# Optimization experiments

Hardware: AMD Instinct MI355X
Metric: run time of the kernel (lower is better)

Reference implementation:

```python
import jax, jax.numpy as jnp
import numpy as np

D = 768
H = 8
DH = D // H
SCALE = DH ** -0.5


def layer_norm(x, g, b, eps=1e-5):
    mu = jnp.mean(x, axis=-1, keepdims=True)
    var = jnp.var(x, axis=-1, keepdims=True)
    return (x - mu) * jax.lax.rsqrt(var + eps) * g + b


def setup_inputs() -> dict:
    key = jax.random.key(0)
    ks = jax.random.split(key, 8)
    B, N = 8, 1024
    s = lambda fan_in: 1.0 / np.sqrt(fan_in)
    return {
        "x": jax.random.normal(ks[0], (B, N, D), jnp.float32),
        "w_qkv": jax.random.normal(ks[1], (D, 3 * D), jnp.float32) * s(D),
        "w_o": jax.random.normal(ks[2], (D, D), jnp.float32) * s(D),
        "b_o": jnp.zeros((D,), jnp.float32),
        "w1": jax.random.normal(ks[3], (D, 4 * D), jnp.float32) * s(D),
        "b1": jnp.zeros((4 * D,), jnp.float32),
        "w2": jax.random.normal(ks[4], (4 * D, D), jnp.float32) * s(4 * D),
        "b2": jnp.zeros((D,), jnp.float32),
        "g1": jnp.ones((D,), jnp.float32), "be1": jnp.zeros((D,), jnp.float32),
        "gm": jnp.ones((D,), jnp.float32), "bm": jnp.zeros((D,), jnp.float32),
        "g3": jnp.ones((D,), jnp.float32), "be3": jnp.zeros((D,), jnp.float32),
    }


def reference(x, w_qkv, w_o, b_o, w1, b1, w2, b2, g1, be1, gm, bm, g3, be3):
    B, N, _ = x.shape
    # --- attention branch (pre-norm) ---
    h = layer_norm(x, g1, be1)
    qkv = h @ w_qkv                                   # (B,N,3D)
    qkv = qkv.reshape(B, N, 3, H, DH).transpose(2, 0, 3, 1, 4)  # (3,B,H,N,Dh)
    q, k, v = qkv[0], qkv[1], qkv[2]
    att = jax.nn.softmax(jnp.einsum('bhnd,bhmd->bhnm', q, k) * SCALE, axis=-1)
    o = jnp.einsum('bhnm,bhmd->bhnd', att, v)         # (B,H,N,Dh)
    # faithful to original: reshape WITHOUT transposing heads back
    o = o.reshape(B, N, D)
    o = o @ w_o + b_o
    x = o + x
    # --- MLP branch (has its own pre-norm; GELU after BOTH linears; dropout off) ---
    h = layer_norm(x, gm, bm)
    h = jax.nn.gelu(h @ w1 + b1, approximate=False)
    h = jax.nn.gelu(h @ w2 + b2, approximate=False)
    x = h + x
    return layer_norm(x, g3, be3)
```

## Files before the change

### kernel.cpp

```cpp
#include <hip/hip_runtime.h>
#include <cmath>
#include <cstdint>

typedef __bf16 bf16;
typedef __bf16 bf16x8 __attribute__((ext_vector_type(8)));
typedef __bf16 bf16x4 __attribute__((ext_vector_type(4)));
typedef float  f32x4  __attribute__((ext_vector_type(4)));

#define M_TOK 8192
#define SCALE_ 0.10206207261596575f

__device__ __forceinline__ void gld_lds16(const void* g, void* l) {
  __builtin_amdgcn_global_load_lds(
      (__attribute__((address_space(1))) void*)(uintptr_t)g,
      (__attribute__((address_space(3))) void*)(uintptr_t)l,
      16, 0, 0);
}

__device__ __forceinline__ float gelu_f(float x) {
  float u = x * (0.7978845608f + 0.0356774081f * x * x);
  float t = 1.0f - 2.0f / (__expf(2.0f * u) + 1.0f);
  return 0.5f * x * (1.0f + t);
}

__global__ __launch_bounds__(256) void transpose_cast_all_kernel(
    const float* __restrict__ w_qkv, const float* __restrict__ w_o,
    const float* __restrict__ w1, const float* __restrict__ w2,
    bf16* __restrict__ wqkvT, bf16* __restrict__ woT, bf16* __restrict__ w1T,
    bf16* __restrict__ w2T) {
  __shared__ float tile[32][33];
  int g = blockIdx.x;
  const float* src;
  bf16* dst;
  int K, N, base, xt;
  if (g < 1728) {
    src = w_qkv; dst = wqkvT; K = 768; N = 2304; base = 0; xt = 72;
  } else if (g < 2304) {
    src = w_o; dst = woT; K = 768; N = 768; base = 1728; xt = 24;
  } else if (g < 4608) {
    src = w1; dst = w1T; K = 768; N = 3072; base = 2304; xt = 96;
  } else {
    src = w2; dst = w2T; K = 3072; N = 768; base = 4608; xt = 24;
  }
  int lid = g - base;
  int nt = (lid % xt) * 32, kt = (lid / xt) * 32;
  int tx = threadIdx.x, ty = threadIdx.y;
#pragma unroll
  for (int i = ty; i < 32; i += 8)
    tile[i][tx] = src[(size_t)(kt + i) * N + nt + tx];
  __syncthreads();
#pragma unroll
  for (int i = ty; i < 32; i += 8)
    dst[(size_t)(nt + i) * K + kt + tx] = (bf16)tile[tx][i];
}

__global__ __launch_bounds__(256) void ln_kernel(
    const float* __restrict__ x, const float* __restrict__ g,
    const float* __restrict__ b, bf16* __restrict__ ob) {
  int w = threadIdx.x >> 6, lane = threadIdx.x & 63;
  size_t row = (size_t)blockIdx.x * 4 + w;
  const float* xr = x + row * 768;
  float4 v[3];
  float s = 0.f, sq = 0.f;
#pragma unroll
  for (int k = 0; k < 3; k++) {
    v[k] = *(const float4*)(xr + (k * 64 + lane) * 4);
    s += v[k].x + v[k].y + v[k].z + v[k].w;
    sq += v[k].x * v[k].x + v[k].y * v[k].y + v[k].z * v[k].z + v[k].w * v[k].w;
  }
#pragma unroll
  for (int off = 32; off >= 1; off >>= 1) {
    s += __shfl_xor(s, off);
    sq += __shfl_xor(sq, off);
  }
  float mean = s * (1.f / 768.f);
  float rstd = rsqrtf(sq * (1.f / 768.f) - mean * mean + 1e-5f);
#pragma unroll
  for (int k = 0; k < 3; k++) {
    int c = (k * 64 + lane) * 4;
    float4 gg = *(const float4*)(g + c);
    float4 bb = *(const float4*)(b + c);
    bf16x4 pk = {(bf16)((v[k].x - mean) * rstd * gg.x + bb.x),
                 (bf16)((v[k].y - mean) * rstd * gg.y + bb.y),
                 (bf16)((v[k].z - mean) * rstd * gg.z + bb.z),
                 (bf16)((v[k].w - mean) * rstd * gg.w + bb.w)};
    *(bf16x4*)(ob + row * 768 + c) = pk;
  }
}

__global__ __launch_bounds__(256) void ln2_reduce_kernel(
    const bf16* __restrict__ p, const float* __restrict__ bo,
    const float* __restrict__ xres, const float* __restrict__ g,
    const float* __restrict__ b, bf16* __restrict__ x2,
    bf16* __restrict__ h2) {
  int w = threadIdx.x >> 6, lane = threadIdx.x & 63;
  size_t row = (size_t)blockIdx.x * 4 + w;
  const bf16* p0 = p + row * 768;
  const bf16* p1 = p0 + (size_t)M_TOK * 768;
  const float* xr = xres + row * 768;
  float4 v[3];
  float s = 0.f, sq = 0.f;
#pragma unroll
  for (int k = 0; k < 3; k++) {
    int c = (k * 64 + lane) * 4;
    bf16x4 a0 = *(const bf16x4*)(p0 + c);
    bf16x4 a1 = *(const bf16x4*)(p1 + c);
    float4 bb = *(const float4*)(bo + c);
    float4 rr = *(const float4*)(xr + c);
    v[k].x = (float)a0[0] + (float)a1[0] + bb.x + rr.x;
    v[k].y = (float)a0[1] + (float)a1[1] + bb.y + rr.y;
    v[k].z = (float)a0[2] + (float)a1[2] + bb.z + rr.z;
    v[k].w = (float)a0[3] + (float)a1[3] + bb.w + rr.w;
    bf16x4 xo = {(bf16)v[k].x, (bf16)v[k].y, (bf16)v[k].z, (bf16)v[k].w};
    *(bf16x4*)(x2 + row * 768 + c) = xo;
    s += v[k].x + v[k].y + v[k].z + v[k].w;
    sq += v[k].x * v[k].x + v[k].y * v[k].y + v[k].z * v[k].z + v[k].w * v[k].w;
  }
#pragma unroll
  for (int off = 32; off >= 1; off >>= 1) {
    s += __shfl_xor(s, off);
    sq += __shfl_xor(sq, off);
  }
  float mean = s * (1.f / 768.f);
  float rstd = rsqrtf(sq * (1.f / 768.f) - mean * mean + 1e-5f);
#pragma unroll
  for (int k = 0; k < 3; k++) {
    int c = (k * 64 + lane) * 4;
    float4 gg = *(const float4*)(g + c);
    float4 bb = *(const float4*)(b + c);
    bf16x4 pk = {(bf16)((v[k].x - mean) * rstd * gg.x + bb.x),
                 (bf16)((v[k].y - mean) * rstd * gg.y + bb.y),
                 (bf16)((v[k].z - mean) * rstd * gg.z + bb.z),
                 (bf16)((v[k].w - mean) * rstd * gg.w + bb.w)};
    *(bf16x4*)(h2 + row * 768 + c) = pk;
  }
}

__global__ __launch_bounds__(256) void ln3_reduce_kernel(
    const bf16* __restrict__ p, const float* __restrict__ b2,
    const bf16* __restrict__ x2, const float* __restrict__ g,
    const float* __restrict__ b, float* __restrict__ out) {
  int w = threadIdx.x >> 6, lane = threadIdx.x & 63;
  size_t row = (size_t)blockIdx.x * 4 + w;
  const bf16* p0 = p + row * 768;
  const bf16* p1 = p0 + (size_t)M_TOK * 768;
  const bf16* xr = x2 + row * 768;
  float4 v[3];
  float s = 0.f, sq = 0.f;
#pragma unroll
  for (int k = 0; k < 3; k++) {
    int c = (k * 64 + lane) * 4;
    bf16x4 a0 = *(const bf16x4*)(p0 + c);
    bf16x4 a1 = *(const bf16x4*)(p1 + c);
    float4 bb = *(const float4*)(b2 + c);
    bf16x4 rr = *(const bf16x4*)(xr + c);
    v[k].x = gelu_f((float)a0[0] + (float)a1[0] + bb.x) + (float)rr[0];
    v[k].y = gelu_f((float)a0[1] + (float)a1[1] + bb.y) + (float)rr[1];
    v[k].z = gelu_f((float)a0[2] + (float)a1[2] + bb.z) + (float)rr[2];
    v[k].w = gelu_f((float)a0[3] + (float)a1[3] + bb.w) + (float)rr[3];
    s += v[k].x + v[k].y + v[k].z + v[k].w;
    sq += v[k].x * v[k].x + v[k].y * v[k].y + v[k].z * v[k].z + v[k].w * v[k].w;
  }
#pragma unroll
  for (int off = 32; off >= 1; off >>= 1) {
    s += __shfl_xor(s, off);
    sq += __shfl_xor(sq, off);
  }
  float mean = s * (1.f / 768.f);
  float rstd = rsqrtf(sq * (1.f / 768.f) - mean * mean + 1e-5f);
#pragma unroll
  for (int k = 0; k < 3; k++) {
    int c = (k * 64 + lane) * 4;
    float4 gg = *(const float4*)(g + c);
    float4 bb = *(const float4*)(b + c);
    float4 ov = {(v[k].x - mean) * rstd * gg.x + bb.x,
                 (v[k].y - mean) * rstd * gg.y + bb.y,
                 (v[k].z - mean) * rstd * gg.z + bb.z,
                 (v[k].w - mean) * rstd * gg.w + bb.w};
    *(float4*)(out + row * 768 + c) = ov;
  }
}

template <int EPI, int LDA, int LDB, int KSL, int NN>
__global__ __launch_bounds__(256) void gemm_bt_kernel(
    const bf16* __restrict__ A, const bf16* __restrict__ Bt,
    const float* __restrict__ bias, bf16* __restrict__ outb,
    bf16* __restrict__ qo, bf16* __restrict__ ko, bf16* __restrict__ vto) {
  __shared__ __align__(16) bf16 As[2][128 * 32];
  __shared__ __align__(16) bf16 Bs[2][128 * 32];
  int tid = threadIdx.x;
  int wave = tid >> 6, lane = tid & 63;
  int qd = lane >> 4, lr = lane & 15;
  int bm0 = blockIdx.y * 128, bn0 = blockIdx.x * 128;
  int wm = (wave >> 1) * 64, wn = (wave & 1) * 64;
  int kbase = blockIdx.z * KSL;

  f32x4 acc[4][4] = {};

  int srow = lane >> 2;
  int scol = ((lane & 3) ^ ((lane >> 3) & 3)) * 8;
  const bf16* Ag = A + (size_t)(bm0 + wave * 32 + srow) * LDA + kbase + scol;
  const bf16* Ag2 = Ag + (size_t)16 * LDA;
  const bf16* Bg = Bt + (size_t)(bn0 + wave * 32 + srow) * LDB + kbase + scol;
  const bf16* Bg2 = Bg + (size_t)16 * LDB;
  int rk = (lr >> 1) & 3;

  auto stage = [&](int k0, int buf) {
    char* Al = (char*)As[buf] + wave * 2048;
    char* Bl = (char*)Bs[buf] + wave * 2048;
    gld_lds16(Ag + k0, Al);
    gld_lds16(Ag2 + k0, Al + 1024);
    gld_lds16(Bg + k0, Bl);
    gld_lds16(Bg2 + k0, Bl + 1024);
  };

  stage(0, 0);
  int cur = 0;
#pragma unroll 4
  for (int k0 = 0; k0 < KSL; k0 += 32) {
    __syncthreads();
    if (k0 + 32 < KSL) stage(k0 + 32, cur ^ 1);
    const bf16* Asr = As[cur];
    const bf16* Bsr = Bs[cur];
    bf16x8 af[4], bfv[4];
#pragma unroll
    for (int i = 0; i < 4; i++)
      af[i] = *(const bf16x8*)&Asr[(wm + i * 16 + lr) * 32 + ((qd ^ rk) * 8)];
#pragma unroll
    for (int j = 0; j < 4; j++)
      bfv[j] = *(const bf16x8*)&Bsr[(wn + j * 16 + lr) * 32 + ((qd ^ rk) * 8)];
#pragma unroll
    for (int i = 0; i < 4; i++)
#pragma unroll
      for (int j = 0; j < 4; j++)
        acc[i][j] = __builtin_amdgcn_mfma_f32_16x16x32_bf16(af[i], bfv[j],
                                                            acc[i][j], 0, 0, 0);
    cur ^= 1;
  }

  bf16* outbs = (EPI == 5) ? outb + (size_t)blockIdx.z * M_TOK * NN : outb;

#pragma unroll
  for (int i = 0; i < 4; i++) {
#pragma unroll
    for (int j = 0; j < 4; j++) {
      if (EPI == 4) {
        int colt = bn0 + wn + j * 16;
        int which = colt / 768;
        int rem = colt - which * 768;
        int h = rem / 96;
        int dhb = rem - h * 96;
        int row0 = bm0 + wm + i * 16 + qd * 4;
        int b = row0 >> 10, n0 = row0 & 1023;
        int bh = b * 8 + h;
        if (which == 2) {
          bf16x4 pk = {(bf16)acc[i][j][0], (bf16)acc[i][j][1],
                       (bf16)acc[i][j][2], (bf16)acc[i][j][3]};
          *(bf16x4*)(vto + ((size_t)(bh * 96 + dhb + lr)) * 1024 + n0) = pk;
        } else if (which == 0) {
#pragma unroll
          for (int r = 0; r < 4; r++)
            qo[((size_t)bh * 1024 + n0 + r) * 96 + dhb + lr] =
                (bf16)(acc[i][j][r] * SCALE_);
        } else {
#pragma unroll
          for (int r = 0; r < 4; r++)
            ko[((size_t)bh * 1024 + n0 + r) * 96 + dhb + lr] =
                (bf16)acc[i][j][r];
        }
      } else {
#pragma unroll
        for (int r = 0; r < 4; r++) {
          int row = bm0 + wm + i * 16 + qd * 4 + r;
          int col = bn0 + wn + j * 16 + lr;
          size_t o = (size_t)row * NN + col;
          float v = acc[i][j][r];
          if (EPI == 2) {
            outbs[o] = (bf16)gelu_f(v + bias[col]);
          } else {
            outbs[o] = (bf16)v;
          }
        }
      }
    }
  }
}

__global__ __launch_bounds__(256) void attn_kernel(
    const bf16* __restrict__ qb, const bf16* __restrict__ kb,
    const bf16* __restrict__ vtb, bf16* __restrict__ operm) {
  __shared__ __align__(16) bf16 Ks[2][64 * 104];
  __shared__ __align__(16) bf16 Vs[2][96 * 72];
  __shared__ __align__(16) bf16 Ps[128 * 72];
  int t = threadIdx.x;
  int w = t >> 6, lane = t & 63;
  int qd = lane >> 4, lr = lane & 15;
  int bh = blockIdx.x, nt0 = blockIdx.y * 128;
  int bq = bh >> 3, hh = bh & 7;

  const bf16* kgb = kb + (size_t)bh * 1024 * 96;
  const bf16* vgb = vtb + (size_t)bh * 96 * 1024;

  bf16x8 kreg[3], vreg[3];
#pragma unroll
  for (int it = 0; it < 3; it++) {
    int idx = it * 256 + t;
    kreg[it] = *(const bf16x8*)(kgb + (idx / 12) * 96 + (idx % 12) * 8);
    vreg[it] = *(const bf16x8*)(vgb + (size_t)(idx >> 3) * 1024 + (idx & 7) * 8);
  }

  const bf16* qg = qb + ((size_t)bh * 1024 + nt0 + w * 32) * 96;
  bf16x8 afq[2][3];
#pragma unroll
  for (int i = 0; i < 2; i++)
#pragma unroll
    for (int ks = 0; ks < 3; ks++)
      afq[i][ks] = *(const bf16x8*)(qg + (i * 16 + lr) * 96 + ks * 32 + qd * 8);

  f32x4 oacc[2][6] = {};
  float lst[2][4] = {};

  int cur = 0;
  for (int kt = 0; kt < 16; kt++) {
#pragma unroll
    for (int it = 0; it < 3; it++) {
      int idx = it * 256 + t;
      *(bf16x8*)&Ks[cur][(idx / 12) * 104 + (idx % 12) * 8] = kreg[it];
      *(bf16x8*)&Vs[cur][(idx >> 3) * 72 + (idx & 7) * 8] = vreg[it];
    }
    if (kt < 15) {
      const bf16* kg = kgb + (size_t)(kt + 1) * 64 * 96;
      const bf16* vg = vgb + (kt + 1) * 64;
#pragma unroll
      for (int it = 0; it < 3; it++) {
        int idx = it * 256 + t;
        kreg[it] = *(const bf16x8*)(kg + (idx / 12) * 96 + (idx % 12) * 8);
        vreg[it] =
            *(const bf16x8*)(vg + (size_t)(idx >> 3) * 1024 + (idx & 7) * 8);
      }
    }
    __syncthreads();

    f32x4 sacc[2][4] = {};
#pragma unroll
    for (int ks = 0; ks < 3; ks++) {
      bf16x8 bk[4];
#pragma unroll
      for (int jn = 0; jn < 4; jn++)
        bk[jn] =
            *(const bf16x8*)&Ks[cur][(jn * 16 + lr) * 104 + ks * 32 + qd * 8];
#pragma unroll
      for (int i = 0; i < 2; i++)
#pragma unroll
        for (int jn = 0; jn < 4; jn++)
          sacc[i][jn] = __builtin_amdgcn_mfma_f32_16x16x32_bf16(
              afq[i][ks], bk[jn], sacc[i][jn], 0, 0, 0);
    }

#pragma unroll
    for (int i = 0; i < 2; i++)
#pragma unroll
      for (int jn = 0; jn < 4; jn++)
#pragma unroll
        for (int r = 0; r < 4; r++) {
          float p = __expf(sacc[i][jn][r]);
          lst[i][r] += p;
          Ps[(w * 32 + i * 16 + qd * 4 + r) * 72 + jn * 16 + lr] = (bf16)p;
        }

#pragma unroll
    for (int ks = 0; ks < 2; ks++) {
      bf16x8 ap[2];
#pragma unroll
      for (int i = 0; i < 2; i++)
        ap[i] =
            *(const bf16x8*)&Ps[(w * 32 + i * 16 + lr) * 72 + ks * 32 + qd * 8];
#pragma unroll
      for (int jn = 0; jn < 6; jn++) {
        bf16x8 bv =
            *(const bf16x8*)&Vs[cur][(jn * 16 + lr) * 72 + ks * 32 + qd * 8];
#pragma unroll
        for (int i = 0; i < 2; i++)
          oacc[i][jn] = __builtin_amdgcn_mfma_f32_16x16x32_bf16(
              ap[i], bv, oacc[i][jn], 0, 0, 0);
      }
    }
    cur ^= 1;
  }

#pragma unroll
  for (int i = 0; i < 2; i++)
#pragma unroll
    for (int r = 0; r < 4; r++) {
#pragma unroll
      for (int off = 1; off < 16; off <<= 1)
        lst[i][r] += __shfl_xor(lst[i][r], off);
    }

#pragma unroll
  for (int i = 0; i < 2; i++) {
#pragma unroll
    for (int r = 0; r < 4; r++) {
      float inv = 1.0f / lst[i][r];
      int n = nt0 + w * 32 + i * 16 + qd * 4 + r;
      size_t rowo = (size_t)bq * 1024 + hh * 128 + (n >> 3);
      int colb = 96 * (n & 7);
#pragma unroll
      for (int jn = 0; jn < 6; jn++)
        operm[rowo * 768 + colb + jn * 16 + lr] =
            (bf16)(oacc[i][jn][r] * inv);
    }
  }
}

extern "C" void kernel_launch(void* const* d_in, const int* in_sizes, int n_in,
                              void* d_out, int out_size, void* d_ws,
                              size_t ws_size, hipStream_t stream) {
  const float* x = (const float*)d_in[0];
  const float* w_qkv = (const float*)d_in[1];
  const float* w_o = (const float*)d_in[2];
  const float* b_o = (const float*)d_in[3];
  const float* w1 = (const float*)d_in[4];
  const float* b1 = (const float*)d_in[5];
  const float* w2 = (const float*)d_in[6];
  const float* b2 = (const float*)d_in[7];
  const float* g1 = (const float*)d_in[8];
  const float* be1 = (const float*)d_in[9];
  const float* gm = (const float*)d_in[10];
  const float* bm = (const float*)d_in[11];
  const float* g3 = (const float*)d_in[12];
  const float* be3 = (const float*)d_in[13];

  char* ws = (char*)d_ws;
  size_t off = 0;
  auto alloc = [&](size_t bytes) {
    char* p = ws + off;
    off += (bytes + 255) & ~(size_t)255;
    return p;
  };
  const size_t SZ_TOK_BF = (size_t)M_TOK * 768 * 2;
  bf16* wqkvT = (bf16*)alloc((size_t)2304 * 768 * 2);
  bf16* woT = (bf16*)alloc((size_t)768 * 768 * 2);
  bf16* w1T = (bf16*)alloc((size_t)3072 * 768 * 2);
  bf16* w2T = (bf16*)alloc((size_t)768 * 3072 * 2);
  bf16* hA = (bf16*)alloc(SZ_TOK_BF);
  bf16* qb = (bf16*)alloc(SZ_TOK_BF);
  bf16* kbuf = (bf16*)alloc(SZ_TOK_BF);
  bf16* vtb = (bf16*)alloc(SZ_TOK_BF);
  bf16* x2 = (bf16*)alloc(SZ_TOK_BF);
  char* G = alloc((size_t)M_TOK * 3072 * 2);
  bf16* operm = hA;
  bf16* h2 = hA;
  bf16* pWo = (bf16*)G;
  bf16* a1 = (bf16*)G;
  bf16* pW2 = hA;

  transpose_cast_all_kernel<<<6912, dim3(32, 8), 0, stream>>>(
      w_qkv, w_o, w1, w2, wqkvT, woT, w1T, w2T);

  ln_kernel<<<M_TOK / 4, 256, 0, stream>>>(x, g1, be1, hA);

  gemm_bt_kernel<4, 768, 768, 768, 2304><<<dim3(18, 64), 256, 0, stream>>>(
      hA, wqkvT, nullptr, nullptr, qb, kbuf, vtb);

  attn_kernel<<<dim3(64, 8), 256, 0, stream>>>(qb, kbuf, vtb, operm);

  gemm_bt_kernel<5, 768, 768, 384, 768><<<dim3(6, 64, 2), 256, 0, stream>>>(
      operm, woT, nullptr, pWo, nullptr, nullptr, nullptr);

  ln2_reduce_kernel<<<M_TOK / 4, 256, 0, stream>>>(pWo, b_o, x, gm, bm, x2, h2);

  gemm_bt_kernel<2, 768, 768, 768, 3072><<<dim3(24, 64), 256, 0, stream>>>(
      h2, w1T, b1, a1, nullptr, nullptr, nullptr);

  gemm_bt_kernel<5, 3072, 3072, 1536, 768><<<dim3(6, 64, 2), 256, 0, stream>>>(
      a1, w2T, nullptr, pW2, nullptr, nullptr, nullptr);

  ln3_reduce_kernel<<<M_TOK / 4, 256, 0, stream>>>(pW2, b2, x2, g3, be3,
                                                   (float*)d_out);
}
```

Before: 391.4 us.

## Prepack weights into MFMA fragment layout and load B directly to registers

The weight preprocessing kernel now writes weights in a per-16-column, per-32-k fragment order that matches the MFMA operand layout. The GEMM loads B fragments straight from global memory into registers, dropping the B LDS staging buffer and its LDS reads. The grid is also swapped so that blockIdx.x walks M, which lets neighbouring blocks share the same weight tiles in cache. The cost is that B global loads are now synchronous, with no LDS double buffering to hide their latency, and the prepack kernel reads the fp32 weights with strided accesses.

```diff
diff --git a/kernel.cpp b/kernel.cpp
--- a/kernel.cpp
+++ b/kernel.cpp
@@ -23,35 +23,35 @@
   return 0.5f * x * (1.0f + t);
 }
 
-__global__ __launch_bounds__(256) void transpose_cast_all_kernel(
+__global__ __launch_bounds__(256) void make_frags_kernel(
     const float* __restrict__ w_qkv, const float* __restrict__ w_o,
     const float* __restrict__ w1, const float* __restrict__ w2,
-    bf16* __restrict__ wqkvT, bf16* __restrict__ woT, bf16* __restrict__ w1T,
-    bf16* __restrict__ w2T) {
-  __shared__ float tile[32][33];
-  int g = blockIdx.x;
+    bf16* __restrict__ fqkv, bf16* __restrict__ fwo, bf16* __restrict__ fw1,
+    bf16* __restrict__ fw2) {
+  int chunk = blockIdx.x * 4 + (threadIdx.x >> 6);
+  int lane = threadIdx.x & 63;
   const float* src;
   bf16* dst;
-  int K, N, base, xt;
-  if (g < 1728) {
-    src = w_qkv; dst = wqkvT; K = 768; N = 2304; base = 0; xt = 72;
-  } else if (g < 2304) {
-    src = w_o; dst = woT; K = 768; N = 768; base = 1728; xt = 24;
-  } else if (g < 4608) {
-    src = w1; dst = w1T; K = 768; N = 3072; base = 2304; xt = 96;
+  int K, N, base;
+  if (chunk < 3456) {
+    src = w_qkv; dst = fqkv; K = 768; N = 2304; base = 0;
+  } else if (chunk < 4608) {
+    src = w_o; dst = fwo; K = 768; N = 768; base = 3456;
+  } else if (chunk < 9216) {
+    src = w1; dst = fw1; K = 768; N = 3072; base = 4608;
   } else {
-    src = w2; dst = w2T; K = 3072; N = 768; base = 4608; xt = 24;
-  }
-  int lid = g - base;
-  int nt = (lid % xt) * 32, kt = (lid / xt) * 32;
-  int tx = threadIdx.x, ty = threadIdx.y;
-#pragma unroll
-  for (int i = ty; i < 32; i += 8)
-    tile[i][tx] = src[(size_t)(kt + i) * N + nt + tx];
-  __syncthreads();
-#pragma unroll
-  for (int i = ty; i < 32; i += 8)
-    dst[(size_t)(nt + i) * K + kt + tx] = (bf16)tile[tx][i];
+    src = w2; dst = fw2; K = 3072; N = 768; base = 9216;
+  }
+  int lid = chunk - base;
+  int kc = K / 32;
+  int n16 = lid / kc, c = lid - n16 * kc;
+  int lr = lane & 15, qd = lane >> 4;
+  int n = n16 * 16 + lr;
+  int k0 = c * 32 + qd * 8;
+  bf16x8 v;
+#pragma unroll
+  for (int e = 0; e < 8; e++) v[e] = (bf16)src[(size_t)(k0 + e) * N + n];
+  *(bf16x8*)&dst[(size_t)lid * 512 + lane * 8] = v;
 }
 
 __global__ __launch_bounds__(256) void ln_kernel(
@@ -181,19 +181,20 @@
   }
 }
 
-template <int EPI, int LDA, int LDB, int KSL, int NN>
+template <int EPI, int LDA, int KT, int KSL, int NN>
 __global__ __launch_bounds__(256) void gemm_bt_kernel(
-    const bf16* __restrict__ A, const bf16* __restrict__ Bt,
+    const bf16* __restrict__ A, const bf16* __restrict__ Bf,
     const float* __restrict__ bias, bf16* __restrict__ outb,
     bf16* __restrict__ qo, bf16* __restrict__ ko, bf16* __restrict__ vto) {
   __shared__ __align__(16) bf16 As[2][128 * 32];
-  __shared__ __align__(16) bf16 Bs[2][128 * 32];
   int tid = threadIdx.x;
   int wave = tid >> 6, lane = tid & 63;
   int qd = lane >> 4, lr = lane & 15;
-  int bm0 = blockIdx.y * 128, bn0 = blockIdx.x * 128;
+  int bm0 = blockIdx.x * 128, bn0 = blockIdx.y * 128;
   int wm = (wave >> 1) * 64, wn = (wave & 1) * 64;
   int kbase = blockIdx.z * KSL;
+  const int STEPS = KSL / 32;
+  const int KC = KT / 32;
 
   f32x4 acc[4][4] = {};
 
@@ -201,39 +202,37 @@
   int scol = ((lane & 3) ^ ((lane >> 3) & 3)) * 8;
   const bf16* Ag = A + (size_t)(bm0 + wave * 32 + srow) * LDA + kbase + scol;
   const bf16* Ag2 = Ag + (size_t)16 * LDA;
-  const bf16* Bg = Bt + (size_t)(bn0 + wave * 32 + srow) * LDB + kbase + scol;
-  const bf16* Bg2 = Bg + (size_t)16 * LDB;
   int rk = (lr >> 1) & 3;
 
-  auto stage = [&](int k0, int buf) {
+  const bf16* Bfb =
+      Bf + ((size_t)((bn0 + wn) >> 4) * KC + (kbase >> 5)) * 512 + lane * 8;
+
+  auto stage = [&](int c, int buf) {
     char* Al = (char*)As[buf] + wave * 2048;
-    char* Bl = (char*)Bs[buf] + wave * 2048;
-    gld_lds16(Ag + k0, Al);
-    gld_lds16(Ag2 + k0, Al + 1024);
-    gld_lds16(Bg + k0, Bl);
-    gld_lds16(Bg2 + k0, Bl + 1024);
+    gld_lds16(Ag + c * 32, Al);
+    gld_lds16(Ag2 + c * 32, Al + 1024);
   };
 
   stage(0, 0);
   int cur = 0;
 #pragma unroll 4
-  for (int k0 = 0; k0 < KSL; k0 += 32) {
+  for (int c = 0; c < STEPS; c++) {
     __syncthreads();
-    if (k0 + 32 < KSL) stage(k0 + 32, cur ^ 1);
+    if (c + 1 < STEPS) stage(c + 1, cur ^ 1);
+    bf16x8 breg[4];
+#pragma unroll
+    for (int jn = 0; jn < 4; jn++)
+      breg[jn] = *(const bf16x8*)(Bfb + ((size_t)jn * KC + c) * 512);
     const bf16* Asr = As[cur];
-    const bf16* Bsr = Bs[cur];
-    bf16x8 af[4], bfv[4];
+    bf16x8 af[4];
 #pragma unroll
     for (int i = 0; i < 4; i++)
       af[i] = *(const bf16x8*)&Asr[(wm + i * 16 + lr) * 32 + ((qd ^ rk) * 8)];
 #pragma unroll
-    for (int j = 0; j < 4; j++)
-      bfv[j] = *(const bf16x8*)&Bsr[(wn + j * 16 + lr) * 32 + ((qd ^ rk) * 8)];
-#pragma unroll
     for (int i = 0; i < 4; i++)
 #pragma unroll
       for (int j = 0; j < 4; j++)
-        acc[i][j] = __builtin_amdgcn_mfma_f32_16x16x32_bf16(af[i], bfv[j],
+        acc[i][j] = __builtin_amdgcn_mfma_f32_16x16x32_bf16(af[i], breg[j],
                                                             acc[i][j], 0, 0, 0);
     cur ^= 1;
   }
@@ -439,10 +438,10 @@
     return p;
   };
   const size_t SZ_TOK_BF = (size_t)M_TOK * 768 * 2;
-  bf16* wqkvT = (bf16*)alloc((size_t)2304 * 768 * 2);
-  bf16* woT = (bf16*)alloc((size_t)768 * 768 * 2);
-  bf16* w1T = (bf16*)alloc((size_t)3072 * 768 * 2);
-  bf16* w2T = (bf16*)alloc((size_t)768 * 3072 * 2);
+  bf16* fqkv = (bf16*)alloc((size_t)2304 * 768 * 2);
+  bf16* fwo = (bf16*)alloc((size_t)768 * 768 * 2);
+  bf16* fw1 = (bf16*)alloc((size_t)3072 * 768 * 2);
+  bf16* fw2 = (bf16*)alloc((size_t)768 * 3072 * 2);
   bf16* hA = (bf16*)alloc(SZ_TOK_BF);
   bf16* qb = (bf16*)alloc(SZ_TOK_BF);
   bf16* kbuf = (bf16*)alloc(SZ_TOK_BF);
@@ -455,26 +454,26 @@
   bf16* a1 = (bf16*)G;
   bf16* pW2 = hA;
 
-  transpose_cast_all_kernel<<<6912, dim3(32, 8), 0, stream>>>(
-      w_qkv, w_o, w1, w2, wqkvT, woT, w1T, w2T);
+  make_frags_kernel<<<3456, 256, 0, stream>>>(w_qkv, w_o, w1, w2, fqkv, fwo,
+                                              fw1, fw2);
 
   ln_kernel<<<M_TOK / 4, 256, 0, stream>>>(x, g1, be1, hA);
 
-  gemm_bt_kernel<4, 768, 768, 768, 2304><<<dim3(18, 64), 256, 0, stream>>>(
-      hA, wqkvT, nullptr, nullptr, qb, kbuf, vtb);
+  gemm_bt_kernel<4, 768, 768, 768, 2304><<<dim3(64, 18), 256, 0, stream>>>(
+      hA, fqkv, nullptr, nullptr, qb, kbuf, vtb);
 
   attn_kernel<<<dim3(64, 8), 256, 0, stream>>>(qb, kbuf, vtb, operm);
 
-  gemm_bt_kernel<5, 768, 768, 384, 768><<<dim3(6, 64, 2), 256, 0, stream>>>(
-      operm, woT, nullptr, pWo, nullptr, nullptr, nullptr);
+  gemm_bt_kernel<5, 768, 768, 384, 768><<<dim3(64, 6, 2), 256, 0, stream>>>(
+      operm, fwo, nullptr, pWo, nullptr, nullptr, nullptr);
 
   ln2_reduce_kernel<<<M_TOK / 4, 256, 0, stream>>>(pWo, b_o, x, gm, bm, x2, h2);
 
-  gemm_bt_kernel<2, 768, 768, 768, 3072><<<dim3(24, 64), 256, 0, stream>>>(
-      h2, w1T, b1, a1, nullptr, nullptr, nullptr);
-
-  gemm_bt_kernel<5, 3072, 3072, 1536, 768><<<dim3(6, 64, 2), 256, 0, stream>>>(
-      a1, w2T, nullptr, pW2, nullptr, nullptr, nullptr);
+  gemm_bt_kernel<2, 768, 768, 768, 3072><<<dim3(64, 24), 256, 0, stream>>>(
+      h2, fw1, b1, a1, nullptr, nullptr, nullptr);
+
+  gemm_bt_kernel<5, 3072, 3072, 1536, 768><<<dim3(64, 6, 2), 256, 0, stream>>>(
+      a1, fw2, nullptr, pW2, nullptr, nullptr, nullptr);
 
   ln3_reduce_kernel<<<M_TOK / 4, 256, 0, stream>>>(pW2, b2, x2, g3, be3,
                                                    (float*)d_out);
```

Result: faster. 361.7 us (-7.6%).
